# Kernel tuning notes

Measured on AMD Instinct MI355X. Metric: run time of the kernel, lower is better.

## Reference

```python
import jax, jax.numpy as jnp
import numpy as np

N_NODES = 100000
N_EDGES = 6400000


def setup_inputs() -> dict:
    key = jax.random.key(0)
    k1, k2, k3, k4, k5, k6 = jax.random.split(key, 6)
    x = jax.random.normal(k1, (N_NODES, 10), dtype=jnp.float32)
    edge_index = jax.random.randint(k2, (2, N_EDGES), 0, N_NODES, dtype=jnp.int64)
    # GCNConv(10,16) and GCNConv(16,2) parameters (glorot-ish scale)
    W1 = jax.random.normal(k3, (10, 16), dtype=jnp.float32) * (1.0 / np.sqrt(10))
    b1 = jnp.zeros((16,), dtype=jnp.float32)
    W2 = jax.random.normal(k4, (16, 2), dtype=jnp.float32) * (1.0 / np.sqrt(16))
    b2 = jnp.zeros((2,), dtype=jnp.float32)
    return {"x": x, "edge_index": edge_index, "W1": W1, "b1": b1, "W2": W2, "b2": b2}


def _gcn_conv(h, src, dst, norm, W, b, n_nodes):
    # PyG GCNConv: linear first, then normalized scatter-add aggregation
    h = h @ W                                   # [N, out]
    msg = h[src] * norm[:, None]                # gather + per-edge scale
    out = jax.ops.segment_sum(msg, dst, num_segments=n_nodes)
    return out + b


def reference(x, edge_index, W1, b1, W2, b2):
    n_nodes = x.shape[0]
    loop = jnp.arange(n_nodes, dtype=edge_index.dtype)
    src = jnp.concatenate([edge_index[0], loop])  # self-loops added (PyG default)
    dst = jnp.concatenate([edge_index[1], loop])
    # symmetric normalization deg^{-1/2} A_hat deg^{-1/2} (deg from target index)
    deg = jax.ops.segment_sum(jnp.ones_like(dst, dtype=x.dtype), dst, num_segments=n_nodes)
    dinv = jnp.where(deg > 0, jax.lax.rsqrt(deg), 0.0)
    norm = dinv[src] * dinv[dst]                 # [E+N]
    h = _gcn_conv(x, src, dst, norm, W1, b1, n_nodes)
    h = jax.nn.relu(h)
    out = _gcn_conv(h, src, dst, norm, W2, b2, n_nodes)
    return out
```

## Files before the change

### kernel.cpp

```cpp
#include <hip/hip_runtime.h>


#define BKT_BITS  8
#define BKT_SZ    256
#define NBK       512
#define NBLKA     256
#define TPB_A     1024
#define DST_SHIFT 24
#define SRC_MASK  0xFFFFFFu

static __device__ __forceinline__ int get_src(const void* ei, int is64, int n_edges, unsigned e) {
    return is64 ? (int)((const long long*)ei)[e] : ((const int*)ei)[e];
}
static __device__ __forceinline__ int get_dst(const void* ei, int is64, int n_edges, unsigned e) {
    return is64 ? (int)((const long long*)ei)[(unsigned)n_edges + e]
                : ((const int*)ei)[(unsigned)n_edges + e];
}

static __global__ void detect64_kernel(const unsigned int* __restrict__ w, int* flag) {
    __shared__ int nz;
    if (threadIdx.x == 0) nz = 0;
    __syncthreads();
    int local = 0;
    for (int k = threadIdx.x; k < 4096; k += blockDim.x)
        if (w[2 * k + 1] != 0u) local = 1;
    if (local) atomicOr(&nz, 1);
    __syncthreads();
    if (threadIdx.x == 0) *flag = (nz == 0) ? 1 : 0;
}

static __global__ void histA_kernel(const void* __restrict__ ei, const int* __restrict__ flag,
                                    unsigned* __restrict__ histA, int n_edges) {
    __shared__ unsigned h[NBK];
    for (int i = threadIdx.x; i < NBK; i += TPB_A) h[i] = 0u;
    __syncthreads();
    const int is64 = *flag;
    unsigned stride = gridDim.x * blockDim.x;
    for (unsigned e = blockIdx.x * blockDim.x + threadIdx.x; e < (unsigned)n_edges; e += stride) {
        int d = get_dst(ei, is64, n_edges, e);
        atomicAdd(&h[(unsigned)d >> BKT_BITS], 1u);
    }
    __syncthreads();
    for (int i = threadIdx.x; i < NBK; i += TPB_A)
        histA[blockIdx.x * NBK + i] = h[i];
}

static __global__ void scan1_kernel(unsigned* __restrict__ histA, unsigned* __restrict__ total) {
    __shared__ unsigned s0[NBLKA], s1[NBLKA];
    const int b = blockIdx.x;
    const int t = threadIdx.x;
    unsigned v = histA[t * NBK + b];
    unsigned* a = s0; unsigned* c = s1;
    a[t] = v;
    __syncthreads();
    for (int off = 1; off < NBLKA; off <<= 1) {
        c[t] = a[t] + (t >= off ? a[t - off] : 0u);
        __syncthreads();
        unsigned* tmp = a; a = c; c = tmp;
    }
    histA[t * NBK + b] = a[t] - v;
    if (t == NBLKA - 1) total[b] = a[NBLKA - 1];
}

static __global__ void scan2_kernel(const unsigned* __restrict__ total,
                                    unsigned* __restrict__ bucket_base) {
    __shared__ unsigned s0[NBK], s1[NBK];
    const int t = threadIdx.x;
    unsigned v = total[t];
    unsigned* a = s0; unsigned* c = s1;
    a[t] = v;
    __syncthreads();
    for (int off = 1; off < NBK; off <<= 1) {
        c[t] = a[t] + (t >= off ? a[t - off] : 0u);
        __syncthreads();
        unsigned* tmp = a; a = c; c = tmp;
    }
    bucket_base[t] = a[t] - v;
}

static __global__ void scatterA_kernel(const void* __restrict__ ei, const int* __restrict__ flag,
                                       const unsigned* __restrict__ histA,
                                       const unsigned* __restrict__ bucket_base,
                                       unsigned* __restrict__ bucketed, int n_edges) {
    __shared__ unsigned cur[NBK];
    for (int i = threadIdx.x; i < NBK; i += TPB_A)
        cur[i] = bucket_base[i] + histA[blockIdx.x * NBK + i];
    __syncthreads();
    const int is64 = *flag;
    unsigned stride = gridDim.x * blockDim.x;
    for (unsigned e = blockIdx.x * blockDim.x + threadIdx.x; e < (unsigned)n_edges; e += stride) {
        unsigned s = (unsigned)get_src(ei, is64, n_edges, e);
        unsigned d = (unsigned)get_dst(ei, is64, n_edges, e);
        unsigned pos = atomicAdd(&cur[d >> BKT_BITS], 1u);
        bucketed[pos] = s | ((d & (BKT_SZ - 1u)) << DST_SHIFT);
    }
}

static __global__ void passB_kernel(const unsigned* __restrict__ bucketed,
                                    const unsigned* __restrict__ total,
                                    const unsigned* __restrict__ bucket_base,
                                    const float* __restrict__ x,
                                    unsigned* __restrict__ csr_src,
                                    unsigned* __restrict__ row_start,
                                    unsigned* __restrict__ cnt,
                                    float* __restrict__ dinv,
                                    float* __restrict__ xs, int n_nodes) {
    const int b = blockIdx.x;
    const int n0 = b << BKT_BITS;
    const int t = threadIdx.x;
    const unsigned base = bucket_base[b];
    const unsigned count = total[b];

    __shared__ unsigned h[BKT_SZ];
    __shared__ unsigned s0[BKT_SZ], s1[BKT_SZ];
    __shared__ unsigned cur[BKT_SZ];
    h[t] = 0u;
    __syncthreads();
    for (unsigned k = t; k < count; k += BKT_SZ)
        atomicAdd(&h[bucketed[base + k] >> DST_SHIFT], 1u);
    __syncthreads();
    unsigned* a = s0; unsigned* c = s1;
    a[t] = h[t];
    __syncthreads();
    for (int off = 1; off < BKT_SZ; off <<= 1) {
        c[t] = a[t] + (t >= off ? a[t - off] : 0u);
        __syncthreads();
        unsigned* tmp = a; a = c; c = tmp;
    }
    unsigned excl = a[t] - h[t];
    cur[t] = excl;
    int n = n0 + t;
    if (n < n_nodes) {
        row_start[n] = base + excl;
        cnt[n] = h[t];
        float di = rsqrtf((float)(h[t] + 1u));
        dinv[n] = di;
        float v[12];
#pragma unroll
        for (int j = 0; j < 10; j++) v[j] = x[(size_t)n * 10 + j] * di;
        v[10] = 0.f; v[11] = 0.f;
        float4* xr = (float4*)(xs + (size_t)n * 12);
        xr[0] = make_float4(v[0], v[1], v[2], v[3]);
        xr[1] = make_float4(v[4], v[5], v[6], v[7]);
        xr[2] = make_float4(v[8], v[9], v[10], v[11]);
    }
    __syncthreads();
    for (unsigned k = t; k < count; k += BKT_SZ) {
        unsigned w = bucketed[base + k];
        unsigned pos = base + atomicAdd(&cur[w >> DST_SHIFT], 1u);
        csr_src[pos] = w & SRC_MASK;
    }
}

static __global__ void node1_kernel(const float* __restrict__ x, const float* __restrict__ dinv,
                                    float* __restrict__ xs, int n_nodes) {
    int i = blockIdx.x * blockDim.x + threadIdx.x;
    if (i >= n_nodes) return;
    float di = dinv[i];
    float v[12];
#pragma unroll
    for (int j = 0; j < 10; j++) v[j] = x[(size_t)i * 10 + j] * di;
    v[10] = 0.f; v[11] = 0.f;
    float4* xr = (float4*)(xs + (size_t)i * 12);
    xr[0] = make_float4(v[0], v[1], v[2], v[3]);
    xr[1] = make_float4(v[4], v[5], v[6], v[7]);
    xr[2] = make_float4(v[8], v[9], v[10], v[11]);
}

static __global__ void gather1_kernel(const unsigned int* __restrict__ row_start,
                                      const unsigned int* __restrict__ cnt,
                                      const unsigned int* __restrict__ csr_src,
                                      const float* __restrict__ xs,
                                      const float* __restrict__ dinv,
                                      const float* __restrict__ W1, const float* __restrict__ b1,
                                      const float* __restrict__ W2,
                                      float* __restrict__ gs, int n_nodes) {
    int w = blockIdx.x * (blockDim.x >> 6) + (threadIdx.x >> 6);
    int lane = threadIdx.x & 63;
    if (w >= n_nodes) return;
    unsigned start = row_start[w];
    unsigned degn = cnt[w];
    float acc[10];
#pragma unroll
    for (int j = 0; j < 10; j++) acc[j] = 0.f;
    const float4* X = (const float4*)xs;
    for (unsigned k = lane; k < degn; k += 64) {
        unsigned s = csr_src[start + k];
        float4 v0 = X[s * 3 + 0];
        float4 v1 = X[s * 3 + 1];
        float4 v2 = X[s * 3 + 2];
        acc[0] += v0.x; acc[1] += v0.y; acc[2] += v0.z; acc[3] += v0.w;
        acc[4] += v1.x; acc[5] += v1.y; acc[6] += v1.z; acc[7] += v1.w;
        acc[8] += v2.x; acc[9] += v2.y;
    }
#pragma unroll
    for (int off = 32; off > 0; off >>= 1) {
#pragma unroll
        for (int j = 0; j < 10; j++) acc[j] += __shfl_xor(acc[j], off);
    }
    float di = dinv[w];
    const float* xsr = xs + (size_t)w * 12;
    float a[10];
#pragma unroll
    for (int j = 0; j < 10; j++) a[j] = (acc[j] + xsr[j]) * di;
    float g0 = 0.f, g1 = 0.f;
    if (lane < 16) {
        float h = b1[lane];
#pragma unroll
        for (int k = 0; k < 10; k++) h = fmaf(a[k], W1[k * 16 + lane], h);
        h = fmaxf(h, 0.f);
        g0 = h * W2[lane * 2 + 0];
        g1 = h * W2[lane * 2 + 1];
    }
#pragma unroll
    for (int off = 8; off > 0; off >>= 1) {
        g0 += __shfl_xor(g0, off);
        g1 += __shfl_xor(g1, off);
    }
    if (lane == 0) {
        gs[(size_t)w * 2 + 0] = g0 * di;
        gs[(size_t)w * 2 + 1] = g1 * di;
    }
}

static __global__ void gather2_kernel(const unsigned int* __restrict__ row_start,
                                      const unsigned int* __restrict__ cnt,
                                      const unsigned int* __restrict__ csr_src,
                                      const float* __restrict__ gs,
                                      const float* __restrict__ dinv,
                                      const float* __restrict__ b2,
                                      float* __restrict__ out, int n_nodes) {
    int w = blockIdx.x * (blockDim.x >> 6) + (threadIdx.x >> 6);
    int lane = threadIdx.x & 63;
    if (w >= n_nodes) return;
    unsigned start = row_start[w];
    unsigned degn = cnt[w];
    float a0 = 0.f, a1 = 0.f;
    const float2* G = (const float2*)gs;
    for (unsigned k = lane; k < degn; k += 64) {
        unsigned s = csr_src[start + k];
        float2 v = G[s];
        a0 += v.x; a1 += v.y;
    }
#pragma unroll
    for (int off = 32; off > 0; off >>= 1) {
        a0 += __shfl_down(a0, off);
        a1 += __shfl_down(a1, off);
    }
    if (lane == 0) {
        float2 self = G[w];
        float di = dinv[w];
        float2 o;
        o.x = fmaf(a0 + self.x, di, b2[0]);
        o.y = fmaf(a1 + self.y, di, b2[1]);
        ((float2*)out)[w] = o;
    }
}

static __global__ void deg_kernel(const void* __restrict__ ei, const int* __restrict__ flag,
                                  unsigned int* __restrict__ cnt, int n_edges) {
    const int is64 = *flag;
    unsigned stride = gridDim.x * blockDim.x;
    for (unsigned e = blockIdx.x * blockDim.x + threadIdx.x; e < (unsigned)n_edges; e += stride) {
        int d = get_dst(ei, is64, n_edges, e);
        atomicAdd(&cnt[d], 1u);
    }
}
static __global__ void alloc_kernel(const unsigned int* __restrict__ cnt,
                                    unsigned int* __restrict__ row_start,
                                    unsigned int* __restrict__ cursor,
                                    unsigned int* __restrict__ gcur,
                                    float* __restrict__ dinv, int n_nodes) {
    __shared__ unsigned wsum[4];
    int i = blockIdx.x * blockDim.x + threadIdx.x;
    int lane = threadIdx.x & 63;
    int wid = threadIdx.x >> 6;
    unsigned d = (i < n_nodes) ? cnt[i] : 0u;
    unsigned scan = d;
#pragma unroll
    for (int off = 1; off < 64; off <<= 1) {
        unsigned t = __shfl_up(scan, off);
        if (lane >= off) scan += t;
    }
    if (lane == 63) wsum[wid] = scan;
    __syncthreads();
    if (threadIdx.x == 0) {
        unsigned s0 = wsum[0], s1 = wsum[1], s2 = wsum[2], s3 = wsum[3];
        unsigned base = atomicAdd(gcur, s0 + s1 + s2 + s3);
        wsum[0] = base;
        wsum[1] = base + s0;
        wsum[2] = base + s0 + s1;
        wsum[3] = base + s0 + s1 + s2;
    }
    __syncthreads();
    if (i < n_nodes) {
        unsigned pos = wsum[wid] + scan - d;
        row_start[i] = pos;
        cursor[i] = pos;
        dinv[i] = rsqrtf((float)(d + 1u));
    }
}
static __global__ void csrfill_kernel(const void* __restrict__ ei, const int* __restrict__ flag,
                                      unsigned int* __restrict__ cursor,
                                      unsigned int* __restrict__ csr_src, int n_edges) {
    const int is64 = *flag;
    unsigned stride = gridDim.x * blockDim.x;
    for (unsigned e = blockIdx.x * blockDim.x + threadIdx.x; e < (unsigned)n_edges; e += stride) {
        int s = get_src(ei, is64, n_edges, e);
        int d = get_dst(ei, is64, n_edges, e);
        unsigned pos = atomicAdd(&cursor[d], 1u);
        csr_src[pos] = (unsigned)s;
    }
}

extern "C" void kernel_launch(void* const* d_in, const int* in_sizes, int n_in,
                              void* d_out, int out_size, void* d_ws, size_t ws_size,
                              hipStream_t stream) {
    const float* x  = (const float*)d_in[0];
    const void*  ei = d_in[1];
    const float* W1 = (const float*)d_in[2];
    const float* b1 = (const float*)d_in[3];
    const float* W2 = (const float*)d_in[4];
    const float* b2 = (const float*)d_in[5];
    float* out = (float*)d_out;

    const int n_nodes = in_sizes[0] / 10;
    const int n_edges = in_sizes[1] / 2;
    (void)n_in; (void)out_size;

    const int nbuckets = (n_nodes + BKT_SZ - 1) >> BKT_BITS;
    const bool pack_ok = (n_nodes <= (1 << DST_SHIFT)) && (nbuckets <= NBK);

    char* p = (char*)d_ws;
    int* flag = (int*)p;
    unsigned* gcur = (unsigned*)(p + 64);
    p += 256;
    unsigned* row_start = (unsigned*)p; p += (size_t)n_nodes * 4;
    unsigned* cnt = (unsigned*)p;       p += (size_t)n_nodes * 4;
    float* dinv = (float*)p;            p += (size_t)n_nodes * 4;
    float* gs = (float*)p;              p += (size_t)n_nodes * 8;
    float* xs = (float*)p;              p += (size_t)n_nodes * 48;
    unsigned* csr_src = (unsigned*)p;   p += (size_t)n_edges * 4;

    const size_t base_bytes = (size_t)(p - (char*)d_ws);
    const size_t need_new = base_bytes + (size_t)NBLKA * NBK * 4 + 2 * (size_t)NBK * 4 + 64 +
                            (size_t)n_edges * 4;
    const size_t need_old = base_bytes + (size_t)n_nodes * 4;

    if (pack_ok && ws_size >= need_new) {
        unsigned* histA = (unsigned*)p;       p += (size_t)NBLKA * NBK * 4;
        unsigned* total = (unsigned*)p;       p += (size_t)NBK * 4;
        unsigned* bucket_base = (unsigned*)p; p += (size_t)NBK * 4 + 64;
        unsigned* bucketed = (unsigned*)p;    p += (size_t)n_edges * 4;

        detect64_kernel<<<1, 256, 0, stream>>>((const unsigned int*)ei, flag);
        histA_kernel<<<NBLKA, TPB_A, 0, stream>>>(ei, flag, histA, n_edges);
        scan1_kernel<<<NBK, NBLKA, 0, stream>>>(histA, total);
        scan2_kernel<<<1, NBK, 0, stream>>>(total, bucket_base);
        scatterA_kernel<<<NBLKA, TPB_A, 0, stream>>>(ei, flag, histA, bucket_base, bucketed, n_edges);
        passB_kernel<<<nbuckets, BKT_SZ, 0, stream>>>(bucketed, total, bucket_base, x, csr_src,
                                                      row_start, cnt, dinv, xs, n_nodes);
        gather1_kernel<<<(n_nodes + 3) / 4, 256, 0, stream>>>(row_start, cnt, csr_src, xs, dinv,
                                                              W1, b1, W2, gs, n_nodes);
        gather2_kernel<<<(n_nodes + 3) / 4, 256, 0, stream>>>(row_start, cnt, csr_src, gs, dinv,
                                                              b2, out, n_nodes);
    } else if (ws_size >= need_old) {
        unsigned* cursor = (unsigned*)p; p += (size_t)n_nodes * 4;

        hipMemsetAsync(d_ws, 0, 256, stream);
        hipMemsetAsync(cnt, 0, (size_t)n_nodes * 4, stream);
        detect64_kernel<<<1, 256, 0, stream>>>((const unsigned int*)ei, flag);
        deg_kernel<<<2048, 256, 0, stream>>>(ei, flag, cnt, n_edges);
        alloc_kernel<<<(n_nodes + 255) / 256, 256, 0, stream>>>(cnt, row_start, cursor, gcur, dinv, n_nodes);
        csrfill_kernel<<<4096, 256, 0, stream>>>(ei, flag, cursor, csr_src, n_edges);
        node1_kernel<<<(n_nodes + 255) / 256, 256, 0, stream>>>(x, dinv, xs, n_nodes);
        gather1_kernel<<<(n_nodes + 3) / 4, 256, 0, stream>>>(row_start, cnt, csr_src, xs, dinv,
                                                              W1, b1, W2, gs, n_nodes);
        gather2_kernel<<<(n_nodes + 3) / 4, 256, 0, stream>>>(row_start, cnt, csr_src, gs, dinv,
                                                              b2, out, n_nodes);
    }
}
```

Before: 242.4 us.

## Use 16-lane groups per node in gathers and pad node features to 64B

Both gather kernels now give each node a 16-lane subgroup instead of a whole 64-lane wavefront, since the average in-degree is about 64. This cuts idle lanes and shortens the shuffle reductions. The scaled feature rows are padded to 16 floats so each row fills an aligned 64-byte segment, and W1/b1/W2 are staged in shared memory. Workspace buffers are aligned to 256 bytes. In exchange, padding raises the feature footprint, and nodes with higher degree loop more times per lane.

```diff
diff --git a/kernel.cpp b/kernel.cpp
--- a/kernel.cpp
+++ b/kernel.cpp
@@ -8,6 +8,7 @@
 #define TPB_A     1024
 #define DST_SHIFT 24
 #define SRC_MASK  0xFFFFFFu
+#define XS_STRIDE 16
 
 static __device__ __forceinline__ int get_src(const void* ei, int is64, int n_edges, unsigned e) {
     return is64 ? (int)((const long long*)ei)[e] : ((const int*)ei)[e];
@@ -135,14 +136,14 @@
         cnt[n] = h[t];
         float di = rsqrtf((float)(h[t] + 1u));
         dinv[n] = di;
-        float v[12];
+        float v[10];
 #pragma unroll
         for (int j = 0; j < 10; j++) v[j] = x[(size_t)n * 10 + j] * di;
-        v[10] = 0.f; v[11] = 0.f;
-        float4* xr = (float4*)(xs + (size_t)n * 12);
+        float4* xr = (float4*)(xs + (size_t)n * XS_STRIDE);
         xr[0] = make_float4(v[0], v[1], v[2], v[3]);
         xr[1] = make_float4(v[4], v[5], v[6], v[7]);
-        xr[2] = make_float4(v[8], v[9], v[10], v[11]);
+        xr[2] = make_float4(v[8], v[9], 0.f, 0.f);
+        xr[3] = make_float4(0.f, 0.f, 0.f, 0.f);
     }
     __syncthreads();
     for (unsigned k = t; k < count; k += BKT_SZ) {
@@ -157,14 +158,14 @@
     int i = blockIdx.x * blockDim.x + threadIdx.x;
     if (i >= n_nodes) return;
     float di = dinv[i];
-    float v[12];
+    float v[10];
 #pragma unroll
     for (int j = 0; j < 10; j++) v[j] = x[(size_t)i * 10 + j] * di;
-    v[10] = 0.f; v[11] = 0.f;
-    float4* xr = (float4*)(xs + (size_t)i * 12);
+    float4* xr = (float4*)(xs + (size_t)i * XS_STRIDE);
     xr[0] = make_float4(v[0], v[1], v[2], v[3]);
     xr[1] = make_float4(v[4], v[5], v[6], v[7]);
-    xr[2] = make_float4(v[8], v[9], v[10], v[11]);
+    xr[2] = make_float4(v[8], v[9], 0.f, 0.f);
+    xr[3] = make_float4(0.f, 0.f, 0.f, 0.f);
 }
 
 static __global__ void gather1_kernel(const unsigned int* __restrict__ row_start,
@@ -175,51 +176,61 @@
                                       const float* __restrict__ W1, const float* __restrict__ b1,
                                       const float* __restrict__ W2,
                                       float* __restrict__ gs, int n_nodes) {
-    int w = blockIdx.x * (blockDim.x >> 6) + (threadIdx.x >> 6);
-    int lane = threadIdx.x & 63;
-    if (w >= n_nodes) return;
-    unsigned start = row_start[w];
-    unsigned degn = cnt[w];
+    __shared__ float sW1[160];
+    __shared__ float sb1[16];
+    __shared__ float sW2[32];
+    for (int k = threadIdx.x; k < 160; k += blockDim.x) sW1[k] = W1[k];
+    if (threadIdx.x < 16) sb1[threadIdx.x] = b1[threadIdx.x];
+    if (threadIdx.x < 32) sW2[threadIdx.x] = W2[threadIdx.x];
+    __syncthreads();
+    int node = blockIdx.x * (blockDim.x >> 4) + (threadIdx.x >> 4);
+    int lg = threadIdx.x & 15;
+    if (node >= n_nodes) return;
+    unsigned start = row_start[node];
+    unsigned degn = cnt[node];
     float acc[10];
 #pragma unroll
     for (int j = 0; j < 10; j++) acc[j] = 0.f;
     const float4* X = (const float4*)xs;
-    for (unsigned k = lane; k < degn; k += 64) {
+    for (unsigned k = lg; k < degn; k += 16) {
         unsigned s = csr_src[start + k];
-        float4 v0 = X[s * 3 + 0];
-        float4 v1 = X[s * 3 + 1];
-        float4 v2 = X[s * 3 + 2];
+        float4 v0 = X[s * 4 + 0];
+        float4 v1 = X[s * 4 + 1];
+        float4 v2 = X[s * 4 + 2];
         acc[0] += v0.x; acc[1] += v0.y; acc[2] += v0.z; acc[3] += v0.w;
         acc[4] += v1.x; acc[5] += v1.y; acc[6] += v1.z; acc[7] += v1.w;
         acc[8] += v2.x; acc[9] += v2.y;
     }
-#pragma unroll
-    for (int off = 32; off > 0; off >>= 1) {
+    if (lg == 0) {
+        float4 v0 = X[(size_t)node * 4 + 0];
+        float4 v1 = X[(size_t)node * 4 + 1];
+        float4 v2 = X[(size_t)node * 4 + 2];
+        acc[0] += v0.x; acc[1] += v0.y; acc[2] += v0.z; acc[3] += v0.w;
+        acc[4] += v1.x; acc[5] += v1.y; acc[6] += v1.z; acc[7] += v1.w;
+        acc[8] += v2.x; acc[9] += v2.y;
+    }
+#pragma unroll
+    for (int off = 8; off > 0; off >>= 1) {
 #pragma unroll
         for (int j = 0; j < 10; j++) acc[j] += __shfl_xor(acc[j], off);
     }
-    float di = dinv[w];
-    const float* xsr = xs + (size_t)w * 12;
-    float a[10];
-#pragma unroll
-    for (int j = 0; j < 10; j++) a[j] = (acc[j] + xsr[j]) * di;
-    float g0 = 0.f, g1 = 0.f;
-    if (lane < 16) {
-        float h = b1[lane];
-#pragma unroll
-        for (int k = 0; k < 10; k++) h = fmaf(a[k], W1[k * 16 + lane], h);
-        h = fmaxf(h, 0.f);
-        g0 = h * W2[lane * 2 + 0];
-        g1 = h * W2[lane * 2 + 1];
-    }
+    float di = dinv[node];
+    float h = sb1[lg];
+#pragma unroll
+    for (int k = 0; k < 10; k++) h = fmaf(acc[k] * di, sW1[k * 16 + lg], h);
+    h = fmaxf(h, 0.f);
+    float g0 = h * sW2[lg * 2 + 0];
+    float g1 = h * sW2[lg * 2 + 1];
 #pragma unroll
     for (int off = 8; off > 0; off >>= 1) {
         g0 += __shfl_xor(g0, off);
         g1 += __shfl_xor(g1, off);
     }
-    if (lane == 0) {
-        gs[(size_t)w * 2 + 0] = g0 * di;
-        gs[(size_t)w * 2 + 1] = g1 * di;
+    if (lg == 0) {
+        float2 o;
+        o.x = g0 * di;
+        o.y = g1 * di;
+        ((float2*)gs)[node] = o;
     }
 }
 
@@ -230,30 +241,32 @@
                                       const float* __restrict__ dinv,
                                       const float* __restrict__ b2,
                                       float* __restrict__ out, int n_nodes) {
-    int w = blockIdx.x * (blockDim.x >> 6) + (threadIdx.x >> 6);
-    int lane = threadIdx.x & 63;
-    if (w >= n_nodes) return;
-    unsigned start = row_start[w];
-    unsigned degn = cnt[w];
+    int node = blockIdx.x * (blockDim.x >> 4) + (threadIdx.x >> 4);
+    int lg = threadIdx.x & 15;
+    if (node >= n_nodes) return;
+    unsigned start = row_start[node];
+    unsigned degn = cnt[node];
     float a0 = 0.f, a1 = 0.f;
     const float2* G = (const float2*)gs;
-    for (unsigned k = lane; k < degn; k += 64) {
-        unsigned s = csr_src[start + k];
-        float2 v = G[s];
+    for (unsigned k = lg; k < degn; k += 16) {
+        float2 v = G[csr_src[start + k]];
         a0 += v.x; a1 += v.y;
     }
-#pragma unroll
-    for (int off = 32; off > 0; off >>= 1) {
-        a0 += __shfl_down(a0, off);
-        a1 += __shfl_down(a1, off);
-    }
-    if (lane == 0) {
-        float2 self = G[w];
-        float di = dinv[w];
+    if (lg == 0) {
+        float2 s = G[node];
+        a0 += s.x; a1 += s.y;
+    }
+#pragma unroll
+    for (int off = 8; off > 0; off >>= 1) {
+        a0 += __shfl_xor(a0, off);
+        a1 += __shfl_xor(a1, off);
+    }
+    if (lg == 0) {
+        float di = dinv[node];
         float2 o;
-        o.x = fmaf(a0 + self.x, di, b2[0]);
-        o.y = fmaf(a1 + self.y, di, b2[1]);
-        ((float2*)out)[w] = o;
+        o.x = fmaf(a0, di, b2[0]);
+        o.y = fmaf(a1, di, b2[1]);
+        ((float2*)out)[node] = o;
     }
 }
 
@@ -313,6 +326,10 @@
     }
 }
 
+static inline char* align_up(char* p, size_t a) {
+    return (char*)(((uintptr_t)p + a - 1) & ~(uintptr_t)(a - 1));
+}
+
 extern "C" void kernel_launch(void* const* d_in, const int* in_sizes, int n_in,
                               void* d_out, int out_size, void* d_ws, size_t ws_size,
                               hipStream_t stream) {
@@ -335,23 +352,26 @@
     int* flag = (int*)p;
     unsigned* gcur = (unsigned*)(p + 64);
     p += 256;
-    unsigned* row_start = (unsigned*)p; p += (size_t)n_nodes * 4;
-    unsigned* cnt = (unsigned*)p;       p += (size_t)n_nodes * 4;
-    float* dinv = (float*)p;            p += (size_t)n_nodes * 4;
-    float* gs = (float*)p;              p += (size_t)n_nodes * 8;
-    float* xs = (float*)p;              p += (size_t)n_nodes * 48;
-    unsigned* csr_src = (unsigned*)p;   p += (size_t)n_edges * 4;
+    unsigned* row_start = (unsigned*)p; p = align_up(p + (size_t)n_nodes * 4, 256);
+    unsigned* cnt = (unsigned*)p;       p = align_up(p + (size_t)n_nodes * 4, 256);
+    float* dinv = (float*)p;            p = align_up(p + (size_t)n_nodes * 4, 256);
+    float* gs = (float*)p;              p = align_up(p + (size_t)n_nodes * 8, 256);
+    float* xs = (float*)p;              p = align_up(p + (size_t)n_nodes * 4 * XS_STRIDE, 256);
+    unsigned* csr_src = (unsigned*)p;   p = align_up(p + (size_t)n_edges * 4, 256);
 
     const size_t base_bytes = (size_t)(p - (char*)d_ws);
-    const size_t need_new = base_bytes + (size_t)NBLKA * NBK * 4 + 2 * (size_t)NBK * 4 + 64 +
+    const size_t need_new = base_bytes + (size_t)NBLKA * NBK * 4 + 2 * (size_t)NBK * 4 + 1024 +
                             (size_t)n_edges * 4;
-    const size_t need_old = base_bytes + (size_t)n_nodes * 4;
+    const size_t need_old = base_bytes + (size_t)n_nodes * 4 + 256;
+
+    const int NODES_PER_BLK = 256 / 16;
+    const int gblocks = (n_nodes + NODES_PER_BLK - 1) / NODES_PER_BLK;
 
     if (pack_ok && ws_size >= need_new) {
-        unsigned* histA = (unsigned*)p;       p += (size_t)NBLKA * NBK * 4;
-        unsigned* total = (unsigned*)p;       p += (size_t)NBK * 4;
-        unsigned* bucket_base = (unsigned*)p; p += (size_t)NBK * 4 + 64;
-        unsigned* bucketed = (unsigned*)p;    p += (size_t)n_edges * 4;
+        unsigned* histA = (unsigned*)p;       p = align_up(p + (size_t)NBLKA * NBK * 4, 256);
+        unsigned* total = (unsigned*)p;       p = align_up(p + (size_t)NBK * 4, 256);
+        unsigned* bucket_base = (unsigned*)p; p = align_up(p + (size_t)NBK * 4, 256);
+        unsigned* bucketed = (unsigned*)p;    p = align_up(p + (size_t)n_edges * 4, 256);
 
         detect64_kernel<<<1, 256, 0, stream>>>((const unsigned int*)ei, flag);
         histA_kernel<<<NBLKA, TPB_A, 0, stream>>>(ei, flag, histA, n_edges);
@@ -360,12 +380,12 @@
         scatterA_kernel<<<NBLKA, TPB_A, 0, stream>>>(ei, flag, histA, bucket_base, bucketed, n_edges);
         passB_kernel<<<nbuckets, BKT_SZ, 0, stream>>>(bucketed, total, bucket_base, x, csr_src,
                                                       row_start, cnt, dinv, xs, n_nodes);
-        gather1_kernel<<<(n_nodes + 3) / 4, 256, 0, stream>>>(row_start, cnt, csr_src, xs, dinv,
-                                                              W1, b1, W2, gs, n_nodes);
-        gather2_kernel<<<(n_nodes + 3) / 4, 256, 0, stream>>>(row_start, cnt, csr_src, gs, dinv,
-                                                              b2, out, n_nodes);
+        gather1_kernel<<<gblocks, 256, 0, stream>>>(row_start, cnt, csr_src, xs, dinv,
+                                                    W1, b1, W2, gs, n_nodes);
+        gather2_kernel<<<gblocks, 256, 0, stream>>>(row_start, cnt, csr_src, gs, dinv,
+                                                    b2, out, n_nodes);
     } else if (ws_size >= need_old) {
-        unsigned* cursor = (unsigned*)p; p += (size_t)n_nodes * 4;
+        unsigned* cursor = (unsigned*)p;
 
         hipMemsetAsync(d_ws, 0, 256, stream);
         hipMemsetAsync(cnt, 0, (size_t)n_nodes * 4, stream);
@@ -374,9 +394,9 @@
         alloc_kernel<<<(n_nodes + 255) / 256, 256, 0, stream>>>(cnt, row_start, cursor, gcur, dinv, n_nodes);
         csrfill_kernel<<<4096, 256, 0, stream>>>(ei, flag, cursor, csr_src, n_edges);
         node1_kernel<<<(n_nodes + 255) / 256, 256, 0, stream>>>(x, dinv, xs, n_nodes);
-        gather1_kernel<<<(n_nodes + 3) / 4, 256, 0, stream>>>(row_start, cnt, csr_src, xs, dinv,
-                                                              W1, b1, W2, gs, n_nodes);
-        gather2_kernel<<<(n_nodes + 3) / 4, 256, 0, stream>>>(row_start, cnt, csr_src, gs, dinv,
-                                                              b2, out, n_nodes);
-    }
-}
+        gather1_kernel<<<gblocks, 256, 0, stream>>>(row_start, cnt, csr_src, xs, dinv,
+                                                    W1, b1, W2, gs, n_nodes);
+        gather2_kernel<<<gblocks, 256, 0, stream>>>(row_start, cnt, csr_src, gs, dinv,
+                                                    b2, out, n_nodes);
+    }
+}
```

Measured after the change: 216.5 us. -10.7%, faster.
